# Performance work log

Measured on AMD Instinct MI355X. Metric: run time of the kernel, lower is better.

Reference implementation:

```python
import jax, jax.numpy as jnp
import numpy as np

N_NODES = 8192
N_EDGES = 262144
D_IN = 512
D_OUT = 512


def setup_inputs() -> dict:
    key = jax.random.key(0)
    k1, k2, k3 = jax.random.split(key, 3)
    x = jax.random.normal(k1, (N_NODES, D_IN), dtype=jnp.float32)
    edge_index = jax.random.randint(k2, (2, N_EDGES), 0, N_NODES, dtype=jnp.int64)
    weight = jax.random.normal(k3, (D_IN, D_OUT), dtype=jnp.float32)
    bias = jnp.zeros((D_OUT,), dtype=jnp.float32)
    return {"x": x, "edge_index": edge_index, "weight": weight, "bias": bias}


def reference(x, edge_index, weight, bias):
    # GCN layer with selfloop=True branch of the original module.
    n = x.shape[0]
    # Dense symmetric adjacency via scatter-set, matching adj[ei0,ei1]=1; adj[ei1,ei0]=1
    adj = jnp.zeros((n, n), dtype=x.dtype)
    adj = adj.at[edge_index[0], edge_index[1]].set(1.0)
    adj = adj.at[edge_index[1], edge_index[0]].set(1.0)
    # Add self loops, symmetric degree normalization D^{-1/2} A D^{-1/2}
    adj = adj + jnp.eye(n, dtype=x.dtype)
    deg = jnp.sum(adj, axis=1)
    dinv = 1.0 / jnp.sqrt(deg)
    adj = adj * dinv[:, None] * dinv[None, :]  # == D @ adj @ D (diagonal scaling)
    return adj @ (x @ weight) + bias
```

## Files before the change

kernel.cpp:

```cpp
#include <hip/hip_runtime.h>
#include <hip/hip_bf16.h>


#define ELL_STRIDE 128

typedef __attribute__((ext_vector_type(8))) short bf16x8;
typedef __attribute__((ext_vector_type(4))) float f32x4;

__device__ __forceinline__ unsigned short f2bf(float f) {
  unsigned u = __float_as_uint(f);
  u = (u + 0x7fff + ((u >> 16) & 1)) >> 16;
  return (unsigned short)u;
}
__device__ __forceinline__ float bflo(unsigned u) {
  return __uint_as_float(u << 16);
}
__device__ __forceinline__ float bfhi(unsigned u) {
  return __uint_as_float(u & 0xffff0000u);
}

__global__ __launch_bounds__(256) void fused_front_kernel(
    const int* __restrict__ ei, unsigned* __restrict__ mask,
    int* __restrict__ degcnt, int n_edges, int words,
    const float* __restrict__ x, unsigned short* __restrict__ xb, int n4,
    const float* __restrict__ W, unsigned short* __restrict__ Wt, int K, int N,
    unsigned short* __restrict__ Hs, int n_nodes,
    int edge_blocks, int cast_blocks, int tr_blocks) {
  const int bid = blockIdx.x;
  if (bid < edge_blocks) {
    const int e = bid * 256 + threadIdx.x;
    if (e < n_edges) {
      const int u = ei[e];
      const int v = ei[e + n_edges];
      const unsigned bv = 1u << (v & 31);
      const unsigned bu = 1u << (u & 31);
      const unsigned o0 = atomicOr(&mask[(size_t)u * words + (v >> 5)], bv);
      if (!(o0 & bv)) atomicAdd(&degcnt[u], 1);
      const unsigned o1 = atomicOr(&mask[(size_t)v * words + (u >> 5)], bu);
      if (!(o1 & bu)) atomicAdd(&degcnt[v], 1);
    }
    return;
  }
  if (bid < edge_blocks + cast_blocks) {
    const int t = (bid - edge_blocks) * 256 + threadIdx.x;
    if (t < n4) {
      float4 v = ((const float4*)x)[t];
      ushort4 o;
      o.x = f2bf(v.x); o.y = f2bf(v.y); o.z = f2bf(v.z); o.w = f2bf(v.w);
      ((ushort4*)xb)[t] = o;
    }
    return;
  }
  if (bid < edge_blocks + cast_blocks + tr_blocks) {
    __shared__ float tile[32][33];
    const int b = bid - edge_blocks - cast_blocks;
    const int bx = b & ((N >> 5) - 1);
    const int by = b >> (31 - __builtin_clz(N >> 5));
    const int tx = threadIdx.x & 31;
    const int ty = threadIdx.x >> 5;
#pragma unroll
    for (int r = 0; r < 4; ++r)
      tile[ty + 8 * r][tx] = W[(size_t)(by * 32 + ty + 8 * r) * N + bx * 32 + tx];
    __syncthreads();
#pragma unroll
    for (int r = 0; r < 4; ++r)
      Wt[(size_t)(bx * 32 + ty + 8 * r) * K + by * 32 + tx] =
          f2bf(tile[tx][ty + 8 * r]);
    return;
  }
  {
    const int t = threadIdx.x;
    if (t < (N >> 1)) ((unsigned*)(Hs + (size_t)n_nodes * N))[t] = 0;
  }
}

__global__ __launch_bounds__(256) void fused_mid_kernel(
    const unsigned short* __restrict__ xb,
    const unsigned short* __restrict__ Wt,
    const int* __restrict__ degcnt,
    unsigned short* __restrict__ Hs,
    const unsigned* __restrict__ mask, unsigned short* __restrict__ ell,
    int M, int N, int K, int words, int gemm_blocks, int nbx_sh) {
  __shared__ unsigned short As[256 * 8];
  __shared__ unsigned short Bs[256 * 8];

  const int tid = threadIdx.x;
  const int bid = blockIdx.x;

  if (bid < gemm_blocks) {
    const int wave = tid >> 6;
    const int lane = tid & 63;
    const int q = lane >> 4;
    const int c = lane & 15;
    const int bx = bid & ((1 << nbx_sh) - 1);
    const int by = bid >> nbx_sh;
    const int m0 = by * 64;
    const int n0 = bx * 64;
    const int wr = wave >> 1, wc = wave & 1;

    f32x4 acc[2][2] = {};

    for (int k0 = 0; k0 < K; k0 += 32) {
      {
        const unsigned short* g =
            xb + (size_t)(m0 + lane) * K + k0 + wave * 8;
        __builtin_amdgcn_global_load_lds(
            (const __attribute__((address_space(1))) void*)g,
            (__attribute__((address_space(3))) void*)(As + wave * 64 * 8), 16, 0, 0);
      }
      {
        const int s = tid;
        const unsigned short* g =
            Wt + (size_t)(n0 + (s >> 2)) * K + k0 + (s & 3) * 8;
        __builtin_amdgcn_global_load_lds(
            (const __attribute__((address_space(1))) void*)g,
            (__attribute__((address_space(3))) void*)(Bs + wave * 64 * 8), 16, 0, 0);
      }
      __syncthreads();

      bf16x8 a[2], b[2];
#pragma unroll
      for (int tm = 0; tm < 2; ++tm) {
        const int row = wr * 32 + tm * 16 + c;
        a[tm] = *(const bf16x8*)(As + (q * 64 + row) * 8);
      }
#pragma unroll
      for (int tn = 0; tn < 2; ++tn) {
        const int n = wc * 32 + tn * 16 + c;
        b[tn] = *(const bf16x8*)(Bs + (n * 4 + q) * 8);
      }
#pragma unroll
      for (int tm = 0; tm < 2; ++tm)
#pragma unroll
        for (int tn = 0; tn < 2; ++tn)
          acc[tm][tn] = __builtin_amdgcn_mfma_f32_16x16x32_bf16(
              a[tm], b[tn], acc[tm][tn], 0, 0, 0);
      __syncthreads();
    }

#pragma unroll
    for (int tm = 0; tm < 2; ++tm) {
#pragma unroll
      for (int r = 0; r < 4; ++r) {
        const int grow = m0 + wr * 32 + tm * 16 + q * 4 + r;
        const float di = rsqrtf((float)degcnt[grow] + 1.0f);
#pragma unroll
        for (int tn = 0; tn < 2; ++tn) {
          const int gcol = n0 + wc * 32 + tn * 16 + c;
          Hs[(size_t)grow * N + gcol] = f2bf(di * acc[tm][tn][r]);
        }
      }
    }
    return;
  }

  {
    const int wave = tid >> 6, lane = tid & 63;
    const int node = (bid - gemm_blocks) * 4 + wave;
    const unsigned* __restrict__ row = mask + (size_t)node * words;
    unsigned short* __restrict__ out = ell + (size_t)node * ELL_STRIDE;

    int running = 0;
    for (int r = 0; r < words; r += 64) {
      const int w = r + lane;
      unsigned bits = row[w];
      const int cnt = __popc(bits);
      int x = cnt;
#pragma unroll
      for (int d = 1; d < 64; d <<= 1) {
        int y = __shfl_up(x, d, 64);
        if (lane >= d) x += y;
      }
      int pos = running + x - cnt;
      while (bits) {
        const int b = __builtin_ctz(bits);
        bits &= bits - 1;
        if (pos < ELL_STRIDE) out[pos] = (unsigned short)((w << 5) + b);
        ++pos;
      }
      running += __shfl(x, 63, 64);
    }
    if (lane == 0) {
      if (running < ELL_STRIDE) out[running] = (unsigned short)M;
      if (running + 1 < ELL_STRIDE) out[running + 1] = (unsigned short)M;
    }
  }
}

__global__ __launch_bounds__(256) void spmm_kernel(
    const unsigned short* __restrict__ ell, const int* __restrict__ degcnt,
    const unsigned short* __restrict__ Hs, const float* __restrict__ bias,
    float* __restrict__ out, int n, int D) {
  __shared__ unsigned short jl[4][ELL_STRIDE];
  const int wave = threadIdx.x >> 6, lane = threadIdx.x & 63;
  const int i = blockIdx.x * 4 + wave;
  const int h = blockIdx.y;
  const int side = lane >> 5, hl = lane & 31;
  const int Dh = D >> 1;

  jl[wave][lane] = ell[(size_t)i * ELL_STRIDE + lane];
  jl[wave][64 + lane] = ell[(size_t)i * ELL_STRIDE + 64 + lane];
  const int dc = degcnt[i];
  const int d = dc < ELL_STRIDE ? dc : ELL_STRIDE;
  const int kmax = (d + 1) & ~1;

  const unsigned short* __restrict__ hb = Hs + h * Dh + hl * 8;
  float acc[8] = {0.f, 0.f, 0.f, 0.f, 0.f, 0.f, 0.f, 0.f};

  {
    const int js = side ? n : i;
    const uint4 hv = *(const uint4*)(hb + (size_t)js * D);
    acc[0] += bflo(hv.x); acc[1] += bfhi(hv.x);
    acc[2] += bflo(hv.y); acc[3] += bfhi(hv.y);
    acc[4] += bflo(hv.z); acc[5] += bfhi(hv.z);
    acc[6] += bflo(hv.w); acc[7] += bfhi(hv.w);
  }
#pragma unroll 8
  for (int k = 0; k < kmax; k += 2) {
    const int j = jl[wave][k + side];
    const uint4 hv = *(const uint4*)(hb + (size_t)j * D);
    acc[0] += bflo(hv.x); acc[1] += bfhi(hv.x);
    acc[2] += bflo(hv.y); acc[3] += bfhi(hv.y);
    acc[4] += bflo(hv.z); acc[5] += bfhi(hv.z);
    acc[6] += bflo(hv.w); acc[7] += bfhi(hv.w);
  }
#pragma unroll
  for (int t = 0; t < 8; ++t) acc[t] += __shfl_xor(acc[t], 32, 64);

  if (side == 0) {
    const float di = rsqrtf((float)dc + 1.0f);
    const float4 b0 = *(const float4*)(bias + h * Dh + hl * 8);
    const float4 b1 = *(const float4*)(bias + h * Dh + hl * 8 + 4);
    float* op = out + (size_t)i * D + h * Dh + hl * 8;
    float4 o0, o1;
    o0.x = di * acc[0] + b0.x; o0.y = di * acc[1] + b0.y;
    o0.z = di * acc[2] + b0.z; o0.w = di * acc[3] + b0.w;
    o1.x = di * acc[4] + b1.x; o1.y = di * acc[5] + b1.y;
    o1.z = di * acc[6] + b1.z; o1.w = di * acc[7] + b1.w;
    *(float4*)op = o0;
    *(float4*)(op + 4) = o1;
  }
}

extern "C" void kernel_launch(void* const* d_in, const int* in_sizes, int n_in,
                              void* d_out, int out_size, void* d_ws, size_t ws_size,
                              hipStream_t stream) {
  const float* x    = (const float*)d_in[0];
  const int*   ei   = (const int*)d_in[1];
  const float* W    = (const float*)d_in[2];
  const float* bias = (const float*)d_in[3];
  float* out = (float*)d_out;

  const int d_out_dim = in_sizes[3];
  const int d_in_dim  = in_sizes[2] / d_out_dim;
  const int n_nodes   = in_sizes[0] / d_in_dim;
  const int n_edges   = in_sizes[1] / 2;
  const int words     = (n_nodes + 31) / 32;

  char* ws = (char*)d_ws;
  size_t off = 0;
  unsigned* mask = (unsigned*)(ws + off); off += (size_t)n_nodes * words * 4;
  int* degcnt    = (int*)(ws + off);      off += (size_t)n_nodes * 4;
  unsigned short* ell = (unsigned short*)(ws + off); off += (size_t)n_nodes * ELL_STRIDE * 2;
  unsigned short* xb  = (unsigned short*)(ws + off); off += (size_t)n_nodes * d_in_dim * 2;
  unsigned short* Wt  = (unsigned short*)(ws + off); off += (size_t)d_in_dim * d_out_dim * 2;
  unsigned short* Hs  = (unsigned short*)(ws + off);
  off += (size_t)(n_nodes + 1) * d_out_dim * 2;

  hipMemsetAsync(mask, 0, (size_t)n_nodes * words * 4 + (size_t)n_nodes * 4, stream);

  const int edge_blocks = (n_edges + 255) / 256;
  const int n4 = n_nodes * d_in_dim / 4;
  const int cast_blocks = (n4 + 255) / 256;
  const int tr_blocks = (d_in_dim / 32) * (d_out_dim / 32);
  fused_front_kernel<<<edge_blocks + cast_blocks + tr_blocks + 1, 256, 0, stream>>>(
      ei, mask, degcnt, n_edges, words, x, xb, n4, W, Wt, d_in_dim, d_out_dim,
      Hs, n_nodes, edge_blocks, cast_blocks, tr_blocks);

  const int nbx = d_out_dim / 64;
  const int nbx_sh = 31 - __builtin_clz(nbx);
  const int gemm_blocks = nbx * (n_nodes / 64);
  const int ell_blocks = n_nodes / 4;
  fused_mid_kernel<<<gemm_blocks + ell_blocks, 256, 0, stream>>>(
      xb, Wt, degcnt, Hs, mask, ell,
      n_nodes, d_out_dim, d_in_dim, words, gemm_blocks, nbx_sh);

  dim3 sgrid(n_nodes / 4, 2);
  spmm_kernel<<<sgrid, 256, 0, stream>>>(ell, degcnt, Hs, bias, out,
                                         n_nodes, d_out_dim);
}
```

Baseline: 168.0 us.

## Derive degree from bitmask popcount and apply column normalization in SpMM

Drops the conditional degree atomics in the edge scatter. Degree is now taken from the popcount pass that builds the ELL lists, which also writes a dinv array. Because the mask pass runs concurrently with the GEMM, the GEMM can no longer prescale rows by dinv. The SpMM gathers dinv[j] per neighbor and scales each row in fp32. This removes atomic contention and the degree memset, at the cost of an extra scalar gather and multiplies per neighbor in the SpMM loop.

```diff
diff --git a/kernel.cpp b/kernel.cpp
--- a/kernel.cpp
+++ b/kernel.cpp
@@ -20,8 +20,8 @@
 }
 
 __global__ __launch_bounds__(256) void fused_front_kernel(
-    const int* __restrict__ ei, unsigned* __restrict__ mask,
-    int* __restrict__ degcnt, int n_edges, int words,
+    const int* __restrict__ ei, unsigned* __restrict__ mask, int n_edges,
+    int words,
     const float* __restrict__ x, unsigned short* __restrict__ xb, int n4,
     const float* __restrict__ W, unsigned short* __restrict__ Wt, int K, int N,
     unsigned short* __restrict__ Hs, int n_nodes,
@@ -32,12 +32,8 @@
     if (e < n_edges) {
       const int u = ei[e];
       const int v = ei[e + n_edges];
-      const unsigned bv = 1u << (v & 31);
-      const unsigned bu = 1u << (u & 31);
-      const unsigned o0 = atomicOr(&mask[(size_t)u * words + (v >> 5)], bv);
-      if (!(o0 & bv)) atomicAdd(&degcnt[u], 1);
-      const unsigned o1 = atomicOr(&mask[(size_t)v * words + (u >> 5)], bu);
-      if (!(o1 & bu)) atomicAdd(&degcnt[v], 1);
+      atomicOr(&mask[(size_t)u * words + (v >> 5)], 1u << (v & 31));
+      atomicOr(&mask[(size_t)v * words + (u >> 5)], 1u << (u & 31));
     }
     return;
   }
@@ -77,9 +73,9 @@
 __global__ __launch_bounds__(256) void fused_mid_kernel(
     const unsigned short* __restrict__ xb,
     const unsigned short* __restrict__ Wt,
-    const int* __restrict__ degcnt,
     unsigned short* __restrict__ Hs,
     const unsigned* __restrict__ mask, unsigned short* __restrict__ ell,
+    int* __restrict__ deg, float* __restrict__ dinv,
     int M, int N, int K, int words, int gemm_blocks, int nbx_sh) {
   __shared__ unsigned short As[256 * 8];
   __shared__ unsigned short Bs[256 * 8];
@@ -88,6 +84,7 @@
   const int bid = blockIdx.x;
 
   if (bid < gemm_blocks) {
+    if (bid == 0 && tid == 0) dinv[M] = 0.f;
     const int wave = tid >> 6;
     const int lane = tid & 63;
     const int q = lane >> 4;
@@ -143,11 +140,10 @@
 #pragma unroll
       for (int r = 0; r < 4; ++r) {
         const int grow = m0 + wr * 32 + tm * 16 + q * 4 + r;
-        const float di = rsqrtf((float)degcnt[grow] + 1.0f);
 #pragma unroll
         for (int tn = 0; tn < 2; ++tn) {
           const int gcol = n0 + wc * 32 + tn * 16 + c;
-          Hs[(size_t)grow * N + gcol] = f2bf(di * acc[tm][tn][r]);
+          Hs[(size_t)grow * N + gcol] = f2bf(acc[tm][tn][r]);
         }
       }
     }
@@ -181,6 +177,9 @@
       running += __shfl(x, 63, 64);
     }
     if (lane == 0) {
+      const int dd = running < ELL_STRIDE ? running : ELL_STRIDE;
+      deg[node] = dd;
+      dinv[node] = rsqrtf((float)running + 1.0f);
       if (running < ELL_STRIDE) out[running] = (unsigned short)M;
       if (running + 1 < ELL_STRIDE) out[running + 1] = (unsigned short)M;
     }
@@ -188,9 +187,9 @@
 }
 
 __global__ __launch_bounds__(256) void spmm_kernel(
-    const unsigned short* __restrict__ ell, const int* __restrict__ degcnt,
-    const unsigned short* __restrict__ Hs, const float* __restrict__ bias,
-    float* __restrict__ out, int n, int D) {
+    const unsigned short* __restrict__ ell, const int* __restrict__ deg,
+    const float* __restrict__ dinv, const unsigned short* __restrict__ Hs,
+    const float* __restrict__ bias, float* __restrict__ out, int n, int D) {
   __shared__ unsigned short jl[4][ELL_STRIDE];
   const int wave = threadIdx.x >> 6, lane = threadIdx.x & 63;
   const int i = blockIdx.x * 4 + wave;
@@ -200,8 +199,8 @@
 
   jl[wave][lane] = ell[(size_t)i * ELL_STRIDE + lane];
   jl[wave][64 + lane] = ell[(size_t)i * ELL_STRIDE + 64 + lane];
-  const int dc = degcnt[i];
-  const int d = dc < ELL_STRIDE ? dc : ELL_STRIDE;
+  const int d = deg[i];
+  const float di = dinv[i];
   const int kmax = (d + 1) & ~1;
 
   const unsigned short* __restrict__ hb = Hs + h * Dh + hl * 8;
@@ -209,26 +208,27 @@
 
   {
     const int js = side ? n : i;
+    const float ds = side ? 0.f : di;
     const uint4 hv = *(const uint4*)(hb + (size_t)js * D);
-    acc[0] += bflo(hv.x); acc[1] += bfhi(hv.x);
-    acc[2] += bflo(hv.y); acc[3] += bfhi(hv.y);
-    acc[4] += bflo(hv.z); acc[5] += bfhi(hv.z);
-    acc[6] += bflo(hv.w); acc[7] += bfhi(hv.w);
+    acc[0] += ds * bflo(hv.x); acc[1] += ds * bfhi(hv.x);
+    acc[2] += ds * bflo(hv.y); acc[3] += ds * bfhi(hv.y);
+    acc[4] += ds * bflo(hv.z); acc[5] += ds * bfhi(hv.z);
+    acc[6] += ds * bflo(hv.w); acc[7] += ds * bfhi(hv.w);
   }
 #pragma unroll 8
   for (int k = 0; k < kmax; k += 2) {
     const int j = jl[wave][k + side];
+    const float dj = dinv[j];
     const uint4 hv = *(const uint4*)(hb + (size_t)j * D);
-    acc[0] += bflo(hv.x); acc[1] += bfhi(hv.x);
-    acc[2] += bflo(hv.y); acc[3] += bfhi(hv.y);
-    acc[4] += bflo(hv.z); acc[5] += bfhi(hv.z);
-    acc[6] += bflo(hv.w); acc[7] += bfhi(hv.w);
+    acc[0] += dj * bflo(hv.x); acc[1] += dj * bfhi(hv.x);
+    acc[2] += dj * bflo(hv.y); acc[3] += dj * bfhi(hv.y);
+    acc[4] += dj * bflo(hv.z); acc[5] += dj * bfhi(hv.z);
+    acc[6] += dj * bflo(hv.w); acc[7] += dj * bfhi(hv.w);
   }
 #pragma unroll
   for (int t = 0; t < 8; ++t) acc[t] += __shfl_xor(acc[t], 32, 64);
 
   if (side == 0) {
-    const float di = rsqrtf((float)dc + 1.0f);
     const float4 b0 = *(const float4*)(bias + h * Dh + hl * 8);
     const float4 b1 = *(const float4*)(bias + h * Dh + hl * 8 + 4);
     float* op = out + (size_t)i * D + h * Dh + hl * 8;
@@ -260,21 +260,22 @@
   char* ws = (char*)d_ws;
   size_t off = 0;
   unsigned* mask = (unsigned*)(ws + off); off += (size_t)n_nodes * words * 4;
-  int* degcnt    = (int*)(ws + off);      off += (size_t)n_nodes * 4;
+  int* deg       = (int*)(ws + off);      off += (size_t)n_nodes * 4;
+  float* dinv    = (float*)(ws + off);    off += (size_t)(n_nodes + 1) * 4;
   unsigned short* ell = (unsigned short*)(ws + off); off += (size_t)n_nodes * ELL_STRIDE * 2;
   unsigned short* xb  = (unsigned short*)(ws + off); off += (size_t)n_nodes * d_in_dim * 2;
   unsigned short* Wt  = (unsigned short*)(ws + off); off += (size_t)d_in_dim * d_out_dim * 2;
   unsigned short* Hs  = (unsigned short*)(ws + off);
   off += (size_t)(n_nodes + 1) * d_out_dim * 2;
 
-  hipMemsetAsync(mask, 0, (size_t)n_nodes * words * 4 + (size_t)n_nodes * 4, stream);
+  hipMemsetAsync(mask, 0, (size_t)n_nodes * words * 4, stream);
 
   const int edge_blocks = (n_edges + 255) / 256;
   const int n4 = n_nodes * d_in_dim / 4;
   const int cast_blocks = (n4 + 255) / 256;
   const int tr_blocks = (d_in_dim / 32) * (d_out_dim / 32);
   fused_front_kernel<<<edge_blocks + cast_blocks + tr_blocks + 1, 256, 0, stream>>>(
-      ei, mask, degcnt, n_edges, words, x, xb, n4, W, Wt, d_in_dim, d_out_dim,
+      ei, mask, n_edges, words, x, xb, n4, W, Wt, d_in_dim, d_out_dim,
       Hs, n_nodes, edge_blocks, cast_blocks, tr_blocks);
 
   const int nbx = d_out_dim / 64;
@@ -282,10 +283,10 @@
   const int gemm_blocks = nbx * (n_nodes / 64);
   const int ell_blocks = n_nodes / 4;
   fused_mid_kernel<<<gemm_blocks + ell_blocks, 256, 0, stream>>>(
-      xb, Wt, degcnt, Hs, mask, ell,
+      xb, Wt, Hs, mask, ell, deg, dinv,
       n_nodes, d_out_dim, d_in_dim, words, gemm_blocks, nbx_sh);
 
   dim3 sgrid(n_nodes / 4, 2);
-  spmm_kernel<<<sgrid, 256, 0, stream>>>(ell, degcnt, Hs, bias, out,
+  spmm_kernel<<<sgrid, 256, 0, stream>>>(ell, deg, dinv, Hs, bias, out,
                                          n_nodes, d_out_dim);
 }
```

Result: faster. 161.0 us (-4.2%).
